# Performance work log

Hardware: AMD Instinct MI355X
Metric: run time of the kernel (lower is better)

## Reference

```python
import jax, jax.numpy as jnp
import numpy as np

NF = 64        # feature channels (nf == inter_channels == in_channels)
BURST = 14     # burst_size from Args
H = 128
W = 128
SCALE = 0.02   # weight init scale keeps softmax logits in a sane range


def conv1x1(x, w, b):
    # x: [B,C,H,W], w: [O,C], b: [O]
    return jnp.einsum('bchw,oc->bohw', x, w) + b[None, :, None, None]


def setup_inputs() -> dict:
    key = jax.random.key(0)
    ks = jax.random.split(key, 32)
    inp = {'aligned_fea': jax.random.normal(ks[0], (BURST, NF, H, W), dtype=jnp.float32)}
    names = ['gc', 'thc', 'phc', 'Wc', 'gh', 'thh', 'phh', 'Wh', 'gw', 'thw', 'phw', 'Ww']
    for i, n in enumerate(names):
        inp[n + '_w'] = SCALE * jax.random.normal(ks[1 + 2 * i], (NF, NF), dtype=jnp.float32)
        inp[n + '_b'] = SCALE * jax.random.normal(ks[2 + 2 * i], (NF,), dtype=jnp.float32)
    inp['fus_w'] = SCALE * jax.random.normal(ks[26], (NF, BURST * NF * 3), dtype=jnp.float32)
    inp['fus_b'] = SCALE * jax.random.normal(ks[27], (NF,), dtype=jnp.float32)
    return inp


def _forward(aligned_fea,
             gc_w, gc_b, thc_w, thc_b, phc_w, phc_b, Wc_w, Wc_b,
             gh_w, gh_b, thh_w, thh_b, phh_w, phh_b, Wh_w, Wh_b,
             gw_w, gw_b, thw_w, thw_b, phw_w, phw_b, Ww_w, Ww_b,
             fus_w, fus_b):
    B, C, h, w = aligned_fea.shape  # [14, 64, 128, 128]
    x = aligned_fea
    ref = aligned_fea[0:1]  # [1,C,H,W]

    # ---- channel non-local (self) ----
    g = conv1x1(x, gc_w, gc_b).reshape(B, C, h * w)
    th = conv1x1(x, thc_w, thc_b).reshape(B, C, h * w)
    ph = conv1x1(x, phc_w, phc_b).reshape(B, C, h * w)
    f = jnp.einsum('bcn,bdn->bcd', th, ph)            # [B,C,C]
    f = jax.nn.softmax(f, axis=1)                     # softmax over dim=1 as in torch
    y = jnp.einsum('bcd,bdn->bcn', f, g)              # [B,C,HW]
    y = jnp.transpose(y, (0, 2, 1)).reshape(B, C, h, w)  # permute+view as in torch
    zc = conv1x1(y, Wc_w, Wc_b) + x

    # ---- height non-local (cross with ref) ----
    g = conv1x1(x, gh_w, gh_b).reshape(B, h, C * w)
    th = conv1x1(ref, thh_w, thh_b).reshape(1, h, C * w)
    ph = conv1x1(x, phh_w, phh_b).reshape(B, h, C * w)
    f = jnp.einsum('bik,bjk->bij', jnp.broadcast_to(th, (B, h, C * w)), ph)  # [B,H,H]
    f = jax.nn.softmax(f, axis=1)
    y = jnp.einsum('bij,bjk->bik', f, g)              # [B,H,C*W]
    y = jnp.transpose(y, (0, 2, 1)).reshape(B, C, h, w)  # requires H == W
    zh = conv1x1(y, Wh_w, Wh_b) + x

    # ---- width non-local (cross with ref) ----
    g = conv1x1(x, gw_w, gw_b).reshape(B, w, C * h)
    th = conv1x1(ref, thw_w, thw_b).reshape(1, w, C * h)
    ph = conv1x1(x, phw_w, phw_b).reshape(B, w, C * h)
    f = jnp.einsum('bik,bjk->bij', jnp.broadcast_to(th, (B, w, C * h)), ph)  # [B,W,W]
    f = jax.nn.softmax(f, axis=1)
    y = jnp.einsum('bij,bjk->bik', f, g)              # [B,W,C*H]
    y = jnp.transpose(y, (0, 2, 1)).reshape(B, C, h, w)
    zw = conv1x1(y, Ww_w, Ww_b) + x

    # ---- fusion: cat frames along channel in order [c, h, w] ----
    feat = jnp.concatenate([zc.reshape(1, B * C, h, w),
                            zh.reshape(1, B * C, h, w),
                            zw.reshape(1, B * C, h, w)], axis=1)  # [1, 3*B*C, H, W]
    out = conv1x1(feat, fus_w, fus_b)
    return jnp.where(out >= 0, out, 0.2 * out)  # LeakyReLU(0.2)


def reference(aligned_fea,
              gc_w, gc_b, thc_w, thc_b, phc_w, phc_b, Wc_w, Wc_b,
              gh_w, gh_b, thh_w, thh_b, phh_w, phh_b, Wh_w, Wh_b,
              gw_w, gw_b, thw_w, thw_b, phw_w, phw_b, Ww_w, Ww_b,
              fus_w, fus_b):
    return _forward(aligned_fea,
                    gc_w, gc_b, thc_w, thc_b, phc_w, phc_b, Wc_w, Wc_b,
                    gh_w, gh_b, thh_w, thh_b, phh_w, phh_b, Wh_w, Wh_b,
                    gw_w, gw_b, thw_w, thw_b, phw_w, phw_b, Ww_w, Ww_b,
                    fus_w, fus_b)
```

## Files before the change

### kernel.cpp

```cpp
#include <hip/hip_runtime.h>

#define NF 64
#define BURST 14
#define NPIX 16384
#define CN (NF * NPIX)
#define LP 72

typedef short bf16x8 __attribute__((ext_vector_type(8)));
typedef float f32x4 __attribute__((ext_vector_type(4)));
typedef unsigned short us4 __attribute__((ext_vector_type(4)));

__device__ inline unsigned short f2bf(float f) {
    unsigned int u = __float_as_uint(f);
    return (unsigned short)((u + 0x7fffu + ((u >> 16) & 1u)) >> 16);
}
__device__ inline float bf2f(unsigned short u) {
    return __uint_as_float(((unsigned int)u) << 16);
}

__global__ __launch_bounds__(256) void cast_x(const float* __restrict__ X,
                                              unsigned short* __restrict__ XB,
                                              unsigned short* __restrict__ XT,
                                              float* __restrict__ S)
{
    __shared__ unsigned short Xs[128][LP];
    __shared__ float red[256];
    const int tid = threadIdx.x;
    const int p0 = blockIdx.x * 128;
    const int b = blockIdx.y;
    const size_t boff = (size_t)b * CN;
#pragma unroll
    for (int i = 0; i < 8; ++i) {
        const int id = tid + 256 * i;
        const int c = id >> 5, p4 = (id & 31) * 4;
        float4 v = *(const float4*)&X[boff + (size_t)c * NPIX + p0 + p4];
        us4 r;
        r.x = f2bf(v.x); r.y = f2bf(v.y); r.z = f2bf(v.z); r.w = f2bf(v.w);
        *(us4*)&XB[boff + (size_t)c * NPIX + p0 + p4] = r;
        Xs[p4 + 0][c] = r.x; Xs[p4 + 1][c] = r.y;
        Xs[p4 + 2][c] = r.z; Xs[p4 + 3][c] = r.w;
    }
    __syncthreads();
#pragma unroll
    for (int i = 0; i < 4; ++i) {
        const int id = tid + 256 * i;
        const int row = id >> 3, c8 = (id & 7) * 8;
        *(bf16x8*)&XT[boff + (size_t)(p0 + row) * 64 + c8] = *(const bf16x8*)&Xs[row][c8];
    }
    {
        const int c = tid & 63, qq = tid >> 6;
        float sv = 0.f;
        for (int pp = qq * 32; pp < qq * 32 + 32; ++pp) sv += bf2f(Xs[pp][c]);
        red[tid] = sv;
        __syncthreads();
        if (tid < 64) {
            const float t = red[tid] + red[64 + tid] + red[128 + tid] + red[192 + tid];
            atomicAdd(&S[(b * 2 + (p0 >= 8192 ? 1 : 0)) * 64 + tid], t);
        }
    }
}

__global__ __launch_bounds__(256) void precompute(
    const float* __restrict__ fus_w, const float* __restrict__ fus_b,
    const float* __restrict__ Wc, const float* __restrict__ bWc,
    const float* __restrict__ Wh, const float* __restrict__ bWh,
    const float* __restrict__ Ww, const float* __restrict__ bWw,
    const float* __restrict__ gcw, const float* __restrict__ ghw,
    const float* __restrict__ gww,
    unsigned short* __restrict__ M16, unsigned short* __restrict__ Wc16,
    float* __restrict__ cb, unsigned short* __restrict__ gT16)
{
    const int blk = blockIdx.x, tid = threadIdx.x;
    if (blk < 42) {
        __shared__ float Fl[64][65];
        __shared__ float Wl[64][65];
        const int g = blk / 14, b = blk % 14;
        const float* Wg = (g == 0) ? Wc : (g == 1) ? Wh : Ww;
#pragma unroll
        for (int i = 0; i < 4; ++i) {
            const int id = tid + 256 * i;
            const int r = id >> 4, c4 = (id & 15) * 4;
            float4 v = *(const float4*)&fus_w[r * 2688 + g * 896 + b * 64 + c4];
            Fl[r][c4] = v.x; Fl[r][c4 + 1] = v.y; Fl[r][c4 + 2] = v.z; Fl[r][c4 + 3] = v.w;
            float4 u = *(const float4*)&Wg[r * 64 + c4];
            Wl[r][c4] = u.x; Wl[r][c4 + 1] = u.y; Wl[r][c4 + 2] = u.z; Wl[r][c4 + 3] = u.w;
        }
        __syncthreads();
        const int o = tid & 63, qq = tid >> 6;
        float s[16];
#pragma unroll
        for (int i = 0; i < 16; ++i) s[i] = 0.f;
        for (int c2 = 0; c2 < 64; ++c2) {
            const float fv = Fl[o][c2];
#pragma unroll
            for (int i = 0; i < 16; ++i) s[i] += fv * Wl[c2][qq * 16 + i];
        }
        unsigned short* Mout = M16 + (size_t)blk * 4096;
#pragma unroll
        for (int i = 0; i < 16; i += 4) {
            us4 r4; r4.x = f2bf(s[i]); r4.y = f2bf(s[i + 1]); r4.z = f2bf(s[i + 2]); r4.w = f2bf(s[i + 3]);
            *(us4*)&Mout[o * 64 + qq * 16 + i] = r4;
        }
    } else if (blk < 98) {
        const int e0 = (blk - 42) * 1024 + tid * 4;
        const int o = e0 / 896, bc = e0 - o * 896;
        float4 a = *(const float4*)&fus_w[o * 2688 + bc];
        float4 b2 = *(const float4*)&fus_w[o * 2688 + 896 + bc];
        float4 c3 = *(const float4*)&fus_w[o * 2688 + 1792 + bc];
        us4 r;
        r.x = f2bf(a.x + b2.x + c3.x); r.y = f2bf(a.y + b2.y + c3.y);
        r.z = f2bf(a.z + b2.z + c3.z); r.w = f2bf(a.w + b2.w + c3.w);
        *(us4*)&Wc16[e0] = r;
    } else if (blk < 106) {
        __shared__ float red[256];
        const int o = (blk - 98) * 8 + (tid >> 5);
        const int lane = tid & 31;
        float s = 0.f;
        for (int t = 0; t < 84; ++t) {
            const int ch = lane + 32 * t;
            const int g = ch / 896, c2 = ch & 63;
            const float bg = (g == 0) ? bWc[c2] : (g == 1) ? bWh[c2] : bWw[c2];
            s += fus_w[o * 2688 + ch] * bg;
        }
        red[tid] = s;
        __syncthreads();
        if (tid < 8) {
            const int oo = (blk - 98) * 8 + tid;
            float t = fus_b[oo];
            for (int i = 0; i < 32; ++i) t += red[tid * 32 + i];
            cb[oo] = t;
        }
    } else {
        const int g = blk - 106;
        const float* wg = (g == 0) ? gcw : (g == 1) ? ghw : gww;
        unsigned short* dst = gT16 + (size_t)g * 4096;
        for (int e = tid; e < 4096; e += 256) {
            const int cp = e >> 6, d = e & 63;
            dst[e] = f2bf(wg[d * 64 + cp]);
        }
    }
}

__global__ __launch_bounds__(256) void gram(
    const unsigned short* __restrict__ XB, float* __restrict__ Gpart)
{
    const int tid = threadIdx.x;
    const int w = tid >> 6, l = tid & 63, lm = l & 15, q = l >> 4;
    const int b = blockIdx.y;
    const int mo = (w & 1) * 32, no = (w >> 1) * 32;
    const unsigned short* P = XB;
    const unsigned short* Q = XB + (size_t)b * CN;
    f32x4 a0[2][2] = {}, a1[2][2] = {}, a2[2][2] = {}, a3[2][2] = {}, a4[2][2] = {};
#pragma unroll 2
    for (int ki = 0; ki < 8; ++ki) {
        const int k = blockIdx.x * 256 + ki * 32 + q * 8;
        bf16x8 p0[2], p1[2], qm0[2], qm1[2], qn0[2], qn1[2];
#pragma unroll
        for (int mi = 0; mi < 2; ++mi) {
            const size_t rm = (size_t)(mo + mi * 16 + lm) * NPIX;
            const size_t rn = (size_t)(no + mi * 16 + lm) * NPIX;
            p0[mi]  = *(const bf16x8*)&P[rm + k];
            p1[mi]  = *(const bf16x8*)&P[rm + 8192 + k];
            qm0[mi] = *(const bf16x8*)&Q[rm + k];
            qm1[mi] = *(const bf16x8*)&Q[rm + 8192 + k];
            qn0[mi] = *(const bf16x8*)&Q[rn + k];
            qn1[mi] = *(const bf16x8*)&Q[rn + 8192 + k];
        }
#pragma unroll
        for (int mi = 0; mi < 2; ++mi)
#pragma unroll
            for (int ni = 0; ni < 2; ++ni) {
                a0[mi][ni] = __builtin_amdgcn_mfma_f32_16x16x32_bf16(qm0[mi], qn0[ni], a0[mi][ni], 0, 0, 0);
                a0[mi][ni] = __builtin_amdgcn_mfma_f32_16x16x32_bf16(qm1[mi], qn1[ni], a0[mi][ni], 0, 0, 0);
                a1[mi][ni] = __builtin_amdgcn_mfma_f32_16x16x32_bf16(p0[mi], qn0[ni], a1[mi][ni], 0, 0, 0);
                a2[mi][ni] = __builtin_amdgcn_mfma_f32_16x16x32_bf16(p0[mi], qn1[ni], a2[mi][ni], 0, 0, 0);
                a3[mi][ni] = __builtin_amdgcn_mfma_f32_16x16x32_bf16(p1[mi], qn0[ni], a3[mi][ni], 0, 0, 0);
                a4[mi][ni] = __builtin_amdgcn_mfma_f32_16x16x32_bf16(p1[mi], qn1[ni], a4[mi][ni], 0, 0, 0);
            }
    }
    float* Gp = Gpart + (size_t)(blockIdx.x * 14 + b) * 5 * 4096;
#define STORE_Z(zidx, ACC)                                                     \
    for (int mi = 0; mi < 2; ++mi)                                             \
        for (int r = 0; r < 4; ++r)                                            \
            for (int ni = 0; ni < 2; ++ni)                                     \
                Gp[zidx * 4096 + (mo + mi * 16 + q * 4 + r) * 64 + no + ni * 16 + lm] = ACC[mi][ni][r];
    STORE_Z(0, a0) STORE_Z(1, a1) STORE_Z(2, a2) STORE_Z(3, a3) STORE_Z(4, a4)
#undef STORE_Z
}

__global__ __launch_bounds__(256) void gram_reduce(
    const float* __restrict__ Gpart, float* __restrict__ G)
{
    const int e = blockIdx.x * 256 + threadIdx.x;
    float s = 0.f;
#pragma unroll
    for (int ks = 0; ks < 32; ++ks) s += Gpart[(size_t)ks * 286720 + e];
    G[e] = s;
}

__global__ __launch_bounds__(256) void sandwich(
    const float* __restrict__ thc_w, const float* __restrict__ phc_w,
    const float* __restrict__ thc_b, const float* __restrict__ phc_b,
    const float* __restrict__ thh_w, const float* __restrict__ phh_w,
    const float* __restrict__ thh_b, const float* __restrict__ phh_b,
    const float* __restrict__ thw_w, const float* __restrict__ phw_w,
    const float* __restrict__ thw_b, const float* __restrict__ phw_b,
    const float* __restrict__ G, const float* __restrict__ S,
    float* __restrict__ f1, float* __restrict__ f2)
{
    __shared__ float Wt[64][65], Wp[64][65], Gl[64][65], Tl[64][65];
    __shared__ float sth[64], sph[64], uu[64], vv[64], btl[64], bpl[64];
    const int b = blockIdx.x, y = blockIdx.y, tid = threadIdx.x;
    const float *Wth_g, *Wph_g, *bth_g, *bph_g, *Gp;
    float* outp; int dl = 0, dp = 0; float Kn;
    if (y == 0) {
        Wth_g = thc_w; Wph_g = phc_w; bth_g = thc_b; bph_g = phc_b;
        Gp = G + (size_t)(b * 5) * 4096; Kn = 16384.f;
        outp = f1 + (size_t)b * 4096;
    } else {
        const int part = (y - 1) / 4, e = (y - 1) & 3;
        dl = e >> 1; dp = e & 1;
        if (part == 0) { Wth_g = thh_w; Wph_g = phh_w; bth_g = thh_b; bph_g = phh_b; }
        else           { Wth_g = thw_w; Wph_g = phw_w; bth_g = thw_b; bph_g = phw_b; }
        Gp = G + (size_t)(b * 5 + 1 + e) * 4096; Kn = 8192.f;
        outp = f2 + (size_t)(part * 14 + b) * 16384;
    }
#pragma unroll
    for (int i = 0; i < 4; ++i) {
        const int id = tid + 256 * i;
        const int r = id >> 4, c4 = (id & 15) * 4;
        float4 v = *(const float4*)&Wth_g[r * 64 + c4];
        Wt[r][c4] = v.x; Wt[r][c4 + 1] = v.y; Wt[r][c4 + 2] = v.z; Wt[r][c4 + 3] = v.w;
        float4 u = *(const float4*)&Wph_g[r * 64 + c4];
        Wp[r][c4] = u.x; Wp[r][c4 + 1] = u.y; Wp[r][c4 + 2] = u.z; Wp[r][c4 + 3] = u.w;
        float4 g = *(const float4*)&Gp[r * 64 + c4];
        Gl[r][c4] = g.x; Gl[r][c4 + 1] = g.y; Gl[r][c4 + 2] = g.z; Gl[r][c4 + 3] = g.w;
    }
    if (tid < 64) {
        if (y == 0) { const float sf = S[b * 128 + tid] + S[b * 128 + 64 + tid]; sth[tid] = sf; sph[tid] = sf; }
        else { sth[tid] = S[dl * 64 + tid]; sph[tid] = S[b * 128 + dp * 64 + tid]; }
        btl[tid] = bth_g[tid]; bpl[tid] = bph_g[tid];
    }
    __syncthreads();
    if (tid < 64) {
        float su = 0.f, sv = 0.f;
        for (int c = 0; c < 64; ++c) { su += Wt[tid][c] * sth[c]; sv += Wp[tid][c] * sph[c]; }
        uu[tid] = su; vv[tid] = sv;
    }
    const int t = tid & 63, qq = tid >> 6;
    float r16[16];
#pragma unroll
    for (int i = 0; i < 16; ++i) r16[i] = 0.f;
    for (int c = 0; c < 64; ++c) {
        const float fv = Wt[t][c];
#pragma unroll
        for (int i = 0; i < 16; ++i) r16[i] += fv * Gl[c][qq * 16 + i];
    }
#pragma unroll
    for (int i = 0; i < 16; ++i) Tl[t][qq * 16 + i] = r16[i];
    __syncthreads();
#pragma unroll
    for (int i = 0; i < 16; ++i) r16[i] = 0.f;
    for (int c = 0; c < 64; ++c) {
        const float tv = Tl[t][c];
#pragma unroll
        for (int i = 0; i < 16; ++i) r16[i] += tv * Wp[qq * 16 + i][c];
    }
    if (y == 0) {
#pragma unroll
        for (int i = 0; i < 16; ++i) {
            const int d = qq * 16 + i;
            outp[t * 64 + d] = r16[i] + uu[t] * bpl[d] + btl[t] * vv[d] + Kn * btl[t] * bpl[d];
        }
    } else {
#pragma unroll
        for (int i = 0; i < 16; ++i) {
            const int tp = qq * 16 + i;
            outp[(2 * t + dl) * 128 + 2 * tp + dp] =
                r16[i] + uu[t] * bpl[tp] + btl[t] * vv[tp] + Kn * btl[t] * bpl[tp];
        }
    }
}

__global__ __launch_bounds__(256) void softmax_all(
    const float* __restrict__ f1, const float* __restrict__ f2,
    const float* __restrict__ gcb, const float* __restrict__ ghb,
    const float* __restrict__ gwb,
    unsigned short* __restrict__ o1, unsigned short* __restrict__ o2d,
    float* __restrict__ B1, float* __restrict__ B2)
{
    __shared__ float red[256];
    __shared__ float mxA[128], invA[128];
    __shared__ float bgl[64];
    const int bx = blockIdx.x, tid = threadIdx.x;
    if (bx < 14) {
        const float* Fb = f1 + (size_t)bx * 4096;
        unsigned short* Ob = o1 + (size_t)bx * 4096;
        if (tid < 64) bgl[tid] = gcb[tid];
        const int d = tid & 63, qq = tid >> 6;
        float mx = -1e30f;
        for (int c = qq * 16; c < qq * 16 + 16; ++c) mx = fmaxf(mx, Fb[c * 64 + d]);
        red[tid] = mx;
        __syncthreads();
        if (tid < 64) mxA[tid] = fmaxf(fmaxf(red[tid], red[64 + tid]), fmaxf(red[128 + tid], red[192 + tid]));
        __syncthreads();
        const float m = mxA[d];
        float s = 0.f;
        for (int c = qq * 16; c < qq * 16 + 16; ++c) s += __expf(Fb[c * 64 + d] - m);
        red[tid] = s;
        __syncthreads();
        if (tid < 64) invA[tid] = 1.f / (red[tid] + red[64 + tid] + red[128 + tid] + red[192 + tid]);
        __syncthreads();
        const int e0 = tid * 16;
        const int d0 = e0 & 63;
        float bp = 0.f;
#pragma unroll
        for (int i = 0; i < 16; i += 4) {
            us4 r4;
            float v0 = __expf(Fb[e0 + i] - mxA[d0 + i]) * invA[d0 + i];
            float v1 = __expf(Fb[e0 + i + 1] - mxA[d0 + i + 1]) * invA[d0 + i + 1];
            float v2 = __expf(Fb[e0 + i + 2] - mxA[d0 + i + 2]) * invA[d0 + i + 2];
            float v3 = __expf(Fb[e0 + i + 3] - mxA[d0 + i + 3]) * invA[d0 + i + 3];
            bp += v0 * bgl[d0 + i] + v1 * bgl[d0 + i + 1] + v2 * bgl[d0 + i + 2] + v3 * bgl[d0 + i + 3];
            r4.x = f2bf(v0); r4.y = f2bf(v1); r4.z = f2bf(v2); r4.w = f2bf(v3);
            *(us4*)&Ob[e0 + i] = r4;
        }
        red[tid] = bp;
        __syncthreads();
        if (tid < 64)
            B1[bx * 64 + tid] = red[tid * 4] + red[tid * 4 + 1] + red[tid * 4 + 2] + red[tid * 4 + 3];
    } else {
        const int idx = bx - 14;
        const float* Fb = f2 + (size_t)idx * 16384;
        if (tid < 64) bgl[tid] = (idx < 14) ? ghb[tid] : gwb[tid];
        const int j = tid & 127, ih = tid >> 7;
        float mx = -1e30f;
        for (int i = ih * 64; i < ih * 64 + 64; ++i) mx = fmaxf(mx, Fb[i * 128 + j]);
        red[tid] = mx;
        __syncthreads();
        if (tid < 128) mxA[tid] = fmaxf(red[tid], red[128 + tid]);
        __syncthreads();
        const float m = mxA[j];
        float s = 0.f;
        for (int i = ih * 64; i < ih * 64 + 64; ++i) s += __expf(Fb[i * 128 + j] - m);
        red[tid] = s;
        __syncthreads();
        if (tid < 128) invA[tid] = 1.f / (red[tid] + red[128 + tid]);
        __syncthreads();
        const int e0 = tid * 64;
        const int irow = tid >> 1;
        const int j0 = e0 & 127;
        unsigned short vt[2][32];
        float bp = 0.f;
        for (int ii = 0; ii < 64; ++ii) {
            const int jj = j0 + ii;
            const float v = __expf(Fb[e0 + ii] - mxA[jj]) * invA[jj];
            bp += v * bgl[jj >> 1];
            vt[jj & 1][ii >> 1] = f2bf(v);
        }
        unsigned short* Od = o2d + (size_t)idx * 16384 + irow * 64 + (j0 >> 1);
#pragma unroll
        for (int dlt = 0; dlt < 2; ++dlt)
#pragma unroll
            for (int ss = 0; ss < 32; ss += 4)
                *(us4*)&Od[dlt * 8192 + ss] = *(us4*)&vt[dlt][ss];
        red[tid] = bp;
        __syncthreads();
        if (tid < 128) B2[idx * 128 + tid] = red[2 * tid] + red[2 * tid + 1];
    }
}

__global__ __launch_bounds__(256) void kmat(
    const unsigned short* __restrict__ f16_1, const unsigned short* __restrict__ f2d,
    const unsigned short* __restrict__ gT16,
    unsigned short* __restrict__ K1, unsigned short* __restrict__ K2)
{
    const int b = blockIdx.x, y = blockIdx.y, tid = threadIdx.x;
    const int w = tid >> 6, l = tid & 63, lm = l & 15, q = l >> 4;
    if (y == 0) {
        const unsigned short* A = f16_1 + (size_t)b * 4096;
        const unsigned short* Bm = gT16;
        const int mo = (w & 1) * 32, no = (w >> 1) * 32;
        f32x4 acc[2][2] = {};
#pragma unroll
        for (int ks = 0; ks < 2; ++ks) {
            const int k = ks * 32 + q * 8;
            bf16x8 a[2], bb[2];
#pragma unroll
            for (int mi = 0; mi < 2; ++mi) a[mi] = *(const bf16x8*)&A[(mo + mi * 16 + lm) * 64 + k];
#pragma unroll
            for (int ni = 0; ni < 2; ++ni) bb[ni] = *(const bf16x8*)&Bm[(no + ni * 16 + lm) * 64 + k];
#pragma unroll
            for (int mi = 0; mi < 2; ++mi)
#pragma unroll
                for (int ni = 0; ni < 2; ++ni)
                    acc[mi][ni] = __builtin_amdgcn_mfma_f32_16x16x32_bf16(a[mi], bb[ni], acc[mi][ni], 0, 0, 0);
        }
        unsigned short* Kp = K1 + (size_t)b * 4096;
#pragma unroll
        for (int mi = 0; mi < 2; ++mi)
#pragma unroll
            for (int r = 0; r < 4; ++r)
#pragma unroll
                for (int ni = 0; ni < 2; ++ni)
                    Kp[(mo + mi * 16 + q * 4 + r) * 64 + no + ni * 16 + lm] = f2bf(acc[mi][ni][r]);
    } else {
        const int part = y - 1;
        const unsigned short* Bm = gT16 + (size_t)(1 + part) * 4096;
        unsigned short* Kp = K2 + (size_t)(part * 14 + b) * 16384;
        for (int dlt = 0; dlt < 2; ++dlt) {
            const unsigned short* A = f2d + (size_t)(part * 14 + b) * 16384 + dlt * 8192;
            const int mo = (w & 1) * 64, no = (w >> 1) * 32;
            f32x4 acc[4][2] = {};
#pragma unroll
            for (int ks = 0; ks < 2; ++ks) {
                const int k = ks * 32 + q * 8;
                bf16x8 a[4], bb[2];
#pragma unroll
                for (int mi = 0; mi < 4; ++mi) a[mi] = *(const bf16x8*)&A[(mo + mi * 16 + lm) * 64 + k];
#pragma unroll
                for (int ni = 0; ni < 2; ++ni) bb[ni] = *(const bf16x8*)&Bm[(no + ni * 16 + lm) * 64 + k];
#pragma unroll
                for (int mi = 0; mi < 4; ++mi)
#pragma unroll
                    for (int ni = 0; ni < 2; ++ni)
                        acc[mi][ni] = __builtin_amdgcn_mfma_f32_16x16x32_bf16(a[mi], bb[ni], acc[mi][ni], 0, 0, 0);
            }
#pragma unroll
            for (int mi = 0; mi < 4; ++mi)
#pragma unroll
                for (int r = 0; r < 4; ++r)
#pragma unroll
                    for (int ni = 0; ni < 2; ++ni)
                        Kp[dlt * 8192 + (mo + mi * 16 + q * 4 + r) * 64 + no + ni * 16 + lm] = f2bf(acc[mi][ni][r]);
        }
    }
}

__global__ __launch_bounds__(256) void pv_all(
    const unsigned short* __restrict__ XT,
    const unsigned short* __restrict__ K1, const float* __restrict__ B1,
    const unsigned short* __restrict__ K2, const float* __restrict__ B2,
    unsigned short* __restrict__ Y1, unsigned short* __restrict__ Y2,
    unsigned short* __restrict__ Y3)
{
    const int tid = threadIdx.x;
    const int w = tid >> 6, l = tid & 63, lm = l & 15, q = l >> 4;
    const int y = blockIdx.y;
    if (y < 14) {
        const int b = y;
        const int p0 = blockIdx.x * 256 + w * 64;
        const unsigned short* Xb = XT + (size_t)b * CN;
        const unsigned short* Kb = K1 + (size_t)b * 4096;
        f32x4 acc[4][4] = {};
#pragma unroll
        for (int ks = 0; ks < 2; ++ks) {
            const int c0 = ks * 32 + q * 8;
            bf16x8 a[4], bb[4];
#pragma unroll
            for (int mi = 0; mi < 4; ++mi) a[mi] = *(const bf16x8*)&Xb[(size_t)(p0 + mi * 16 + lm) * 64 + c0];
#pragma unroll
            for (int ni = 0; ni < 4; ++ni) bb[ni] = *(const bf16x8*)&Kb[(ni * 16 + lm) * 64 + c0];
#pragma unroll
            for (int mi = 0; mi < 4; ++mi)
#pragma unroll
                for (int ni = 0; ni < 4; ++ni)
                    acc[mi][ni] = __builtin_amdgcn_mfma_f32_16x16x32_bf16(a[mi], bb[ni], acc[mi][ni], 0, 0, 0);
        }
        unsigned short* Yb = Y1 + (size_t)b * CN;
#pragma unroll
        for (int mi = 0; mi < 4; ++mi)
#pragma unroll
            for (int r = 0; r < 4; ++r) {
                const int p = p0 + mi * 16 + q * 4 + r;
#pragma unroll
                for (int ni = 0; ni < 4; ++ni) {
                    const int c = ni * 16 + lm;
                    Yb[(size_t)p * 64 + c] = f2bf(acc[mi][ni][r] + B1[b * 64 + c]);
                }
            }
    } else {
        const int idx = y - 14;
        const int part = idx / 14, b = idx % 14;
        const int k00 = (blockIdx.x >> 1) * 256 + w * 64;
        const int i0 = (blockIdx.x & 1) * 64;
        const unsigned short* Xb = XT + (size_t)b * CN;
        const unsigned short* Kb = K2 + (size_t)(part * 14 + b) * 16384;
        const float* Bb = B2 + (part * 14 + b) * 128;
        f32x4 acc[4][4] = {};
#pragma unroll
        for (int dlt = 0; dlt < 2; ++dlt) {
#pragma unroll
            for (int ks = 0; ks < 2; ++ks) {
                const int c0 = ks * 32 + q * 8;
                bf16x8 a[4], bb[4];
#pragma unroll
                for (int mi = 0; mi < 4; ++mi)
                    a[mi] = *(const bf16x8*)&Xb[(size_t)(dlt * 8192 + k00 + mi * 16 + lm) * 64 + c0];
#pragma unroll
                for (int ni = 0; ni < 4; ++ni)
                    bb[ni] = *(const bf16x8*)&Kb[dlt * 8192 + (i0 + ni * 16 + lm) * 64 + c0];
#pragma unroll
                for (int mi = 0; mi < 4; ++mi)
#pragma unroll
                    for (int ni = 0; ni < 4; ++ni)
                        acc[mi][ni] = __builtin_amdgcn_mfma_f32_16x16x32_bf16(a[mi], bb[ni], acc[mi][ni], 0, 0, 0);
            }
        }
        unsigned short* Yb = (part ? Y3 : Y2) + (size_t)b * CN;
#pragma unroll
        for (int mi = 0; mi < 4; ++mi)
#pragma unroll
            for (int r = 0; r < 4; ++r) {
                const int k = k00 + mi * 16 + q * 4 + r;
#pragma unroll
                for (int ni = 0; ni < 4; ++ni) {
                    const int ii = i0 + ni * 16 + lm;
                    Yb[(size_t)k * 128 + ii] = f2bf(acc[mi][ni][r] + Bb[ii]);
                }
            }
    }
}

__global__ __launch_bounds__(256) void yfold4(
    const unsigned short* __restrict__ M16,
    const unsigned short* __restrict__ Wcomb,
    const unsigned short* __restrict__ Y1, const unsigned short* __restrict__ Y2,
    const unsigned short* __restrict__ Y3, const unsigned short* __restrict__ XT,
    float* __restrict__ Out)
{
    __shared__ unsigned short As[64][LP];
    __shared__ unsigned short Ss[128][LP];
    const int tid = threadIdx.x;
    const int z = blockIdx.z;
    const unsigned short* S = (z == 0) ? Y1 : (z == 1) ? Y2 : (z == 2) ? Y3 : XT;
    const int p0 = blockIdx.x * 128;
    const int t0 = blockIdx.y * 7;
    const int w = tid >> 6, l = tid & 63, lm = l & 15, q = l >> 4;
    const int mo = (w & 1) * 32;
    const int no = (w >> 1) * 64;
    f32x4 acc[2][4] = {};

    for (int t = t0; t < t0 + 7; ++t) {
        __syncthreads();
        if (z < 3) {
            const unsigned short* Ap = M16 + (size_t)(z * 14 + t) * 4096;
#pragma unroll
            for (int i = 0; i < 2; ++i) {
                const int ch = tid + 256 * i;
                const int row = ch >> 3, c8 = (ch & 7) * 8;
                *(bf16x8*)&As[row][c8] = *(const bf16x8*)&Ap[row * 64 + c8];
            }
#pragma unroll
            for (int i = 0; i < 4; ++i) {
                const int id = tid + 256 * i;
                const int c = id & 63, p8 = (id >> 6) * 8;
                bf16x8 v = *(const bf16x8*)&S[(size_t)t * CN + (size_t)c * NPIX + p0 + p8];
#pragma unroll
                for (int j = 0; j < 8; ++j) Ss[p8 + j][c] = (unsigned short)v[j];
            }
        } else {
#pragma unroll
            for (int i = 0; i < 2; ++i) {
                const int ch = tid + 256 * i;
                const int row = ch >> 3, c8 = (ch & 7) * 8;
                *(bf16x8*)&As[row][c8] = *(const bf16x8*)&Wcomb[row * 896 + t * 64 + c8];
            }
#pragma unroll
            for (int i = 0; i < 4; ++i) {
                const int id = tid + 256 * i;
                const int row = id >> 3, c8 = (id & 7) * 8;
                *(bf16x8*)&Ss[row][c8] = *(const bf16x8*)&S[(size_t)t * CN + (size_t)(p0 + row) * 64 + c8];
            }
        }
        __syncthreads();
#pragma unroll
        for (int ks = 0; ks < 2; ++ks) {
            const int c0 = ks * 32 + q * 8;
            bf16x8 a[2], bb[4];
#pragma unroll
            for (int mi = 0; mi < 2; ++mi) a[mi] = *(const bf16x8*)&As[mo + mi * 16 + lm][c0];
#pragma unroll
            for (int ni = 0; ni < 4; ++ni) bb[ni] = *(const bf16x8*)&Ss[no + ni * 16 + lm][c0];
#pragma unroll
            for (int mi = 0; mi < 2; ++mi)
#pragma unroll
                for (int ni = 0; ni < 4; ++ni)
                    acc[mi][ni] = __builtin_amdgcn_mfma_f32_16x16x32_bf16(a[mi], bb[ni], acc[mi][ni], 0, 0, 0);
        }
    }
#pragma unroll
    for (int mi = 0; mi < 2; ++mi)
#pragma unroll
        for (int r = 0; r < 4; ++r) {
            const int o = mo + mi * 16 + q * 4 + r;
#pragma unroll
            for (int ni = 0; ni < 4; ++ni)
                atomicAdd(&Out[(size_t)o * NPIX + p0 + no + ni * 16 + lm], acc[mi][ni][r]);
        }
}

__global__ __launch_bounds__(256) void leaky_cb(float* __restrict__ O, const float* __restrict__ cb)
{
    const int i = blockIdx.x * 256 + threadIdx.x;
    float4 v = ((float4*)O)[i];
    const float b = cb[(i * 4) >> 14];
    v.x += b; v.y += b; v.z += b; v.w += b;
    v.x = v.x >= 0.f ? v.x : 0.2f * v.x;
    v.y = v.y >= 0.f ? v.y : 0.2f * v.y;
    v.z = v.z >= 0.f ? v.z : 0.2f * v.z;
    v.w = v.w >= 0.f ? v.w : 0.2f * v.w;
    ((float4*)O)[i] = v;
}

extern "C" void kernel_launch(void* const* d_in, const int* in_sizes, int n_in,
                              void* d_out, int out_size, void* d_ws, size_t ws_size,
                              hipStream_t stream)
{
    const float* x     = (const float*)d_in[0];
    const float* gc_w  = (const float*)d_in[1];
    const float* gc_b  = (const float*)d_in[2];
    const float* thc_w = (const float*)d_in[3];
    const float* thc_b = (const float*)d_in[4];
    const float* phc_w = (const float*)d_in[5];
    const float* phc_b = (const float*)d_in[6];
    const float* Wc_w  = (const float*)d_in[7];
    const float* Wc_b  = (const float*)d_in[8];
    const float* gh_w  = (const float*)d_in[9];
    const float* gh_b  = (const float*)d_in[10];
    const float* thh_w = (const float*)d_in[11];
    const float* thh_b = (const float*)d_in[12];
    const float* phh_w = (const float*)d_in[13];
    const float* phh_b = (const float*)d_in[14];
    const float* Wh_w  = (const float*)d_in[15];
    const float* Wh_b  = (const float*)d_in[16];
    const float* gw_w  = (const float*)d_in[17];
    const float* gw_b  = (const float*)d_in[18];
    const float* thw_w = (const float*)d_in[19];
    const float* thw_b = (const float*)d_in[20];
    const float* phw_w = (const float*)d_in[21];
    const float* phw_b = (const float*)d_in[22];
    const float* Ww_w  = (const float*)d_in[23];
    const float* Ww_b  = (const float*)d_in[24];
    const float* fus_w = (const float*)d_in[25];
    const float* fus_b = (const float*)d_in[26];

    float* out = (float*)d_out;

    char* p = (char*)d_ws;
    unsigned short* xb   = (unsigned short*)p; p += (size_t)BURST * CN * 2;
    unsigned short* xT   = (unsigned short*)p; p += (size_t)BURST * CN * 2;
    unsigned short* y1   = (unsigned short*)p; p += (size_t)BURST * CN * 2;
    unsigned short* y2   = (unsigned short*)p; p += (size_t)BURST * CN * 2;
    unsigned short* y3   = (unsigned short*)p; p += (size_t)BURST * CN * 2;
    float*          Gbuf = (float*)p;          p += (size_t)BURST * 5 * 4096 * 4;
    float*          sbuf = (float*)p;          p += (size_t)BURST * 2 * 64 * 4;
    float*          f1b  = (float*)p;          p += (size_t)BURST * 4096 * 4;
    float*          f2b  = (float*)p;          p += (size_t)2 * BURST * 16384 * 4;
    unsigned short* f16_1 = (unsigned short*)p; p += (size_t)BURST * 4096 * 2;
    unsigned short* f2d  = (unsigned short*)p; p += (size_t)2 * BURST * 16384 * 2;
    unsigned short* K1   = (unsigned short*)p; p += (size_t)BURST * 4096 * 2;
    unsigned short* K2   = (unsigned short*)p; p += (size_t)2 * BURST * 16384 * 2;
    float*          B1   = (float*)p;          p += (size_t)BURST * 64 * 4;
    float*          B2   = (float*)p;          p += (size_t)2 * BURST * 128 * 4;
    unsigned short* M16  = (unsigned short*)p; p += (size_t)42 * 4096 * 2;
    unsigned short* Wc16 = (unsigned short*)p; p += (size_t)64 * 896 * 2;
    unsigned short* gT16 = (unsigned short*)p; p += (size_t)3 * 4096 * 2;
    float*          cbv  = (float*)p;          p += 256;

    float* Gpart = (float*)y1;

    hipMemsetAsync(sbuf, 0, (size_t)BURST * 2 * 64 * 4, stream);
    hipMemsetAsync(out, 0, (size_t)NF * NPIX * 4, stream);

    cast_x<<<dim3(128, 14), 256, 0, stream>>>(x, xb, xT, sbuf);
    precompute<<<109, 256, 0, stream>>>(fus_w, fus_b, Wc_w, Wc_b, Wh_w, Wh_b, Ww_w, Ww_b,
                                        gc_w, gh_w, gw_w, M16, Wc16, cbv, gT16);
    gram<<<dim3(32, 14), 256, 0, stream>>>(xb, Gpart);
    gram_reduce<<<1120, 256, 0, stream>>>(Gpart, Gbuf);
    sandwich<<<dim3(14, 9), 256, 0, stream>>>(
        thc_w, phc_w, thc_b, phc_b, thh_w, phh_w, thh_b, phh_b,
        thw_w, phw_w, thw_b, phw_b, Gbuf, sbuf, f1b, f2b);
    softmax_all<<<42, 256, 0, stream>>>(f1b, f2b, gc_b, gh_b, gw_b,
                                        f16_1, f2d, B1, B2);
    kmat<<<dim3(14, 3), 256, 0, stream>>>(f16_1, f2d, gT16, K1, K2);
    pv_all<<<dim3(64, 42), 256, 0, stream>>>(xT, K1, B1, K2, B2, y1, y2, y3);
    yfold4<<<dim3(128, 2, 4), 256, 0, stream>>>(M16, Wc16, y1, y2, y3, xT, out);
    leaky_cb<<<1024, 256, 0, stream>>>(out, cbv);
}
```

Before: 331.4 us.

## Transpose pv_all MFMA operands for vectorized stores and fold sbuf memset into precompute

```diff
diff --git a/kernel.cpp b/kernel.cpp
--- a/kernel.cpp
+++ b/kernel.cpp
@@ -68,7 +68,8 @@
     const float* __restrict__ gcw, const float* __restrict__ ghw,
     const float* __restrict__ gww,
     unsigned short* __restrict__ M16, unsigned short* __restrict__ Wc16,
-    float* __restrict__ cb, unsigned short* __restrict__ gT16)
+    float* __restrict__ cb, unsigned short* __restrict__ gT16,
+    float* __restrict__ sbuf)
 {
     const int blk = blockIdx.x, tid = threadIdx.x;
     if (blk < 42) {
@@ -130,7 +131,7 @@
             for (int i = 0; i < 32; ++i) t += red[tid * 32 + i];
             cb[oo] = t;
         }
-    } else {
+    } else if (blk < 109) {
         const int g = blk - 106;
         const float* wg = (g == 0) ? gcw : (g == 1) ? ghw : gww;
         unsigned short* dst = gT16 + (size_t)g * 4096;
@@ -138,6 +139,8 @@
             const int cp = e >> 6, d = e & 63;
             dst[e] = f2bf(wg[d * 64 + cp]);
         }
+    } else {
+        for (int e = tid; e < BURST * 2 * 64; e += 256) sbuf[e] = 0.f;
     }
 }
 
@@ -447,61 +450,67 @@
     const int tid = threadIdx.x;
     const int w = tid >> 6, l = tid & 63, lm = l & 15, q = l >> 4;
     const int y = blockIdx.y;
+    const int mo = (w & 1) * 32;
+    const int nho = (w >> 1) * 64;
     if (y < 14) {
         const int b = y;
-        const int p0 = blockIdx.x * 256 + w * 64;
+        const int pb = blockIdx.x * 128 + nho;
         const unsigned short* Xb = XT + (size_t)b * CN;
         const unsigned short* Kb = K1 + (size_t)b * 4096;
-        f32x4 acc[4][4] = {};
+        f32x4 acc[2][4] = {};
 #pragma unroll
         for (int ks = 0; ks < 2; ++ks) {
             const int c0 = ks * 32 + q * 8;
-            bf16x8 a[4], bb[4];
-#pragma unroll
-            for (int mi = 0; mi < 4; ++mi) a[mi] = *(const bf16x8*)&Xb[(size_t)(p0 + mi * 16 + lm) * 64 + c0];
-#pragma unroll
-            for (int ni = 0; ni < 4; ++ni) bb[ni] = *(const bf16x8*)&Kb[(ni * 16 + lm) * 64 + c0];
-#pragma unroll
-            for (int mi = 0; mi < 4; ++mi)
+            bf16x8 a[2], bb[4];
+#pragma unroll
+            for (int mi = 0; mi < 2; ++mi) a[mi] = *(const bf16x8*)&Kb[(mo + mi * 16 + lm) * 64 + c0];
+#pragma unroll
+            for (int ni = 0; ni < 4; ++ni) bb[ni] = *(const bf16x8*)&Xb[(size_t)(pb + ni * 16 + lm) * 64 + c0];
+#pragma unroll
+            for (int mi = 0; mi < 2; ++mi)
 #pragma unroll
                 for (int ni = 0; ni < 4; ++ni)
                     acc[mi][ni] = __builtin_amdgcn_mfma_f32_16x16x32_bf16(a[mi], bb[ni], acc[mi][ni], 0, 0, 0);
         }
         unsigned short* Yb = Y1 + (size_t)b * CN;
 #pragma unroll
-        for (int mi = 0; mi < 4; ++mi)
-#pragma unroll
-            for (int r = 0; r < 4; ++r) {
-                const int p = p0 + mi * 16 + q * 4 + r;
-#pragma unroll
-                for (int ni = 0; ni < 4; ++ni) {
-                    const int c = ni * 16 + lm;
-                    Yb[(size_t)p * 64 + c] = f2bf(acc[mi][ni][r] + B1[b * 64 + c]);
-                }
-            }
+        for (int mi = 0; mi < 2; ++mi) {
+            const int cbase = mo + mi * 16 + q * 4;
+            const float4 bv = *(const float4*)&B1[b * 64 + cbase];
+#pragma unroll
+            for (int ni = 0; ni < 4; ++ni) {
+                const int p = pb + ni * 16 + lm;
+                us4 r4;
+                r4.x = f2bf(acc[mi][ni][0] + bv.x);
+                r4.y = f2bf(acc[mi][ni][1] + bv.y);
+                r4.z = f2bf(acc[mi][ni][2] + bv.z);
+                r4.w = f2bf(acc[mi][ni][3] + bv.w);
+                *(us4*)&Yb[(size_t)p * 64 + cbase] = r4;
+            }
+        }
     } else {
         const int idx = y - 14;
         const int part = idx / 14, b = idx % 14;
-        const int k00 = (blockIdx.x >> 1) * 256 + w * 64;
         const int i0 = (blockIdx.x & 1) * 64;
+        const int kb = (blockIdx.x >> 1) * 128 + nho;
         const unsigned short* Xb = XT + (size_t)b * CN;
         const unsigned short* Kb = K2 + (size_t)(part * 14 + b) * 16384;
         const float* Bb = B2 + (part * 14 + b) * 128;
-        f32x4 acc[4][4] = {};
+        f32x4 acc[2][4] = {};
 #pragma unroll
         for (int dlt = 0; dlt < 2; ++dlt) {
 #pragma unroll
             for (int ks = 0; ks < 2; ++ks) {
                 const int c0 = ks * 32 + q * 8;
-                bf16x8 a[4], bb[4];
-#pragma unroll
-                for (int mi = 0; mi < 4; ++mi)
-                    a[mi] = *(const bf16x8*)&Xb[(size_t)(dlt * 8192 + k00 + mi * 16 + lm) * 64 + c0];
+                bf16x8 a[2], bb[4];
+#pragma unroll
+                for (int mi = 0; mi < 2; ++mi)
+                    a[mi] = *(const bf16x8*)&Kb[dlt * 8192 + (i0 + mo + mi * 16 + lm) * 64 + c0];
 #pragma unroll
                 for (int ni = 0; ni < 4; ++ni)
-                    bb[ni] = *(const bf16x8*)&Kb[dlt * 8192 + (i0 + ni * 16 + lm) * 64 + c0];
-#pragma unroll
-                for (int mi = 0; mi < 4; ++mi)
+                    bb[ni] = *(const bf16x8*)&Xb[(size_t)(dlt * 8192 + kb + ni * 16 + lm) * 64 + c0];
+#pragma unroll
+                for (int mi = 0; mi < 2; ++mi)
 #pragma unroll
                     for (int ni = 0; ni < 4; ++ni)
                         acc[mi][ni] = __builtin_amdgcn_mfma_f32_16x16x32_bf16(a[mi], bb[ni], acc[mi][ni], 0, 0, 0);
@@ -509,16 +518,20 @@
         }
         unsigned short* Yb = (part ? Y3 : Y2) + (size_t)b * CN;
 #pragma unroll
-        for (int mi = 0; mi < 4; ++mi)
-#pragma unroll
-            for (int r = 0; r < 4; ++r) {
-                const int k = k00 + mi * 16 + q * 4 + r;
-#pragma unroll
-                for (int ni = 0; ni < 4; ++ni) {
-                    const int ii = i0 + ni * 16 + lm;
-                    Yb[(size_t)k * 128 + ii] = f2bf(acc[mi][ni][r] + Bb[ii]);
-                }
-            }
+        for (int mi = 0; mi < 2; ++mi) {
+            const int ibase = i0 + mo + mi * 16 + q * 4;
+            const float4 bv = *(const float4*)&Bb[ibase];
+#pragma unroll
+            for (int ni = 0; ni < 4; ++ni) {
+                const int k = kb + ni * 16 + lm;
+                us4 r4;
+                r4.x = f2bf(acc[mi][ni][0] + bv.x);
+                r4.y = f2bf(acc[mi][ni][1] + bv.y);
+                r4.z = f2bf(acc[mi][ni][2] + bv.z);
+                r4.w = f2bf(acc[mi][ni][3] + bv.w);
+                *(us4*)&Yb[(size_t)k * 128 + ibase] = r4;
+            }
+        }
     }
 }
 
@@ -670,12 +683,11 @@
 
     float* Gpart = (float*)y1;
 
-    hipMemsetAsync(sbuf, 0, (size_t)BURST * 2 * 64 * 4, stream);
     hipMemsetAsync(out, 0, (size_t)NF * NPIX * 4, stream);
 
+    precompute<<<110, 256, 0, stream>>>(fus_w, fus_b, Wc_w, Wc_b, Wh_w, Wh_b, Ww_w, Ww_b,
+                                        gc_w, gh_w, gw_w, M16, Wc16, cbv, gT16, sbuf);
     cast_x<<<dim3(128, 14), 256, 0, stream>>>(x, xb, xT, sbuf);
-    precompute<<<109, 256, 0, stream>>>(fus_w, fus_b, Wc_w, Wc_b, Wh_w, Wh_b, Ww_w, Ww_b,
-                                        gc_w, gh_w, gw_w, M16, Wc16, cbv, gT16);
     gram<<<dim3(32, 14), 256, 0, stream>>>(xb, Gpart);
     gram_reduce<<<1120, 256, 0, stream>>>(Gpart, Gbuf);
     sandwich<<<dim3(14, 9), 256, 0, stream>>>(
@@ -684,7 +696,7 @@
     softmax_all<<<42, 256, 0, stream>>>(f1b, f2b, gc_b, gh_b, gw_b,
                                         f16_1, f2d, B1, B2);
     kmat<<<dim3(14, 3), 256, 0, stream>>>(f16_1, f2d, gT16, K1, K2);
-    pv_all<<<dim3(64, 42), 256, 0, stream>>>(xT, K1, B1, K2, B2, y1, y2, y3);
+    pv_all<<<dim3(128, 42), 256, 0, stream>>>(xT, K1, B1, K2, B2, y1, y2, y3);
     yfold4<<<dim3(128, 2, 4), 256, 0, stream>>>(M16, Wc16, y1, y2, y3, xT, out);
     leaky_cb<<<1024, 256, 0, stream>>>(out, cbv);
 }
```

Result: no change. 337.4 us (+1.8%).
